# Kernel optimization log

Hardware: AMD Instinct MI355X
Metric: run time of the kernel (lower is better)

Reference implementation:

```python
import jax, jax.numpy as jnp
import numpy as np

D_MODEL = 2048
NUM_HEADS = 16
D_K = D_MODEL // NUM_HEADS
B, S = 2, 2048


def setup_inputs() -> dict:
    key = jax.random.key(0)
    ks = jax.random.split(key, 9)
    sc = 1.0 / np.sqrt(D_MODEL)
    x = jax.random.normal(ks[0], (B, S, D_MODEL), dtype=jnp.float32)
    # broadcastable causal mask [1,1,S,S]; mask==0 positions get -inf
    mask = jnp.tril(jnp.ones((S, S), dtype=jnp.int32))[None, None]
    wq = jax.random.normal(ks[1], (D_MODEL, D_MODEL), dtype=jnp.float32) * sc
    bq = jax.random.normal(ks[2], (D_MODEL,), dtype=jnp.float32) * 0.01
    wk = jax.random.normal(ks[3], (D_MODEL, D_MODEL), dtype=jnp.float32) * sc
    bk = jax.random.normal(ks[4], (D_MODEL,), dtype=jnp.float32) * 0.01
    wv = jax.random.normal(ks[5], (D_MODEL, D_MODEL), dtype=jnp.float32) * sc
    bv = jax.random.normal(ks[6], (D_MODEL,), dtype=jnp.float32) * 0.01
    wo = jax.random.normal(ks[7], (D_MODEL, D_MODEL), dtype=jnp.float32) * sc
    bo = jax.random.normal(ks[8], (D_MODEL,), dtype=jnp.float32) * 0.01
    return {"x": x, "wq": wq, "bq": bq, "wk": wk, "bk": bk,
            "wv": wv, "bv": bv, "wo": wo, "bo": bo, "mask": mask}


def reference(x, wq, bq, wk, bk, wv, bv, wo, bo, mask):
    b, s, _ = x.shape
    # nn.Linear computes x @ W.T + b; weights stored [out, in]
    def proj(w, bias):
        y = jnp.einsum('bsd,ed->bse', x, w) + bias
        return y.reshape(b, s, NUM_HEADS, D_K).transpose(0, 2, 1, 3)  # [b,h,s,dk]
    q = proj(wq, bq)
    k = proj(wk, bk)
    v = proj(wv, bv)
    scores = jnp.einsum('bhid,bhjd->bhij', q, k) / jnp.sqrt(jnp.float32(D_K))
    scores = jnp.where(mask == 0, -jnp.inf, scores)
    attn = jax.nn.softmax(scores, axis=-1)  # dropout p=0.0 -> identity
    out = jnp.einsum('bhij,bhjd->bhid', attn, v)
    out = out.transpose(0, 2, 1, 3).reshape(b, s, D_MODEL)
    return jnp.einsum('bsd,ed->bse', out, wo) + bo
```

## Files before the change

kernel.cpp:

```cpp
#include <hip/hip_runtime.h>
#include <cstdint>
#include <cstddef>

typedef __attribute__((ext_vector_type(8))) short bf16x8;
typedef __attribute__((ext_vector_type(8))) unsigned short u16x8;
typedef __attribute__((ext_vector_type(4))) unsigned short u16x4;
typedef __attribute__((ext_vector_type(2))) unsigned u32x2;
typedef __attribute__((ext_vector_type(4))) float f32x4;

#define MFMA16(A, B, C) __builtin_amdgcn_mfma_f32_16x16x32_bf16((A), (B), (C), 0, 0, 0)

__device__ __forceinline__ unsigned short f2bf(float f) {
  unsigned u = __builtin_bit_cast(unsigned, f);
  u += 0x7FFFu + ((u >> 16) & 1u);
  return (unsigned short)(u >> 16);
}
__device__ __forceinline__ unsigned packbf2(float lo, float hi) {
  unsigned ul = __builtin_bit_cast(unsigned, lo);
  unsigned uh = __builtin_bit_cast(unsigned, hi);
  ul += 0x7FFFu + ((ul >> 16) & 1u);
  uh += 0x7FFFu + ((uh >> 16) & 1u);
  return (ul >> 16) | (uh & 0xffff0000u);
}

__device__ __forceinline__ void gload_lds16(const void* gsrc, void* ldst) {
  __builtin_amdgcn_global_load_lds(
      (const __attribute__((address_space(1))) unsigned int*)gsrc,
      (__attribute__((address_space(3))) unsigned int*)ldst,
      16, 0, 0);
}

__global__ __launch_bounds__(256) void cvt_all(
    const float* __restrict__ sx, const float* __restrict__ s1,
    const float* __restrict__ s2, const float* __restrict__ s3,
    const float* __restrict__ s4,
    unsigned short* __restrict__ dx, unsigned short* __restrict__ d1,
    unsigned short* __restrict__ d2, unsigned short* __restrict__ d3,
    unsigned short* __restrict__ d4) {
  const int y = blockIdx.y;
  const float* src;
  unsigned short* dst;
  if (y == 0)      { src = sx;               dst = dx; }
  else if (y == 1) { src = sx + (1u << 22);  dst = dx + (1u << 22); }
  else if (y == 2) { src = s1; dst = d1; }
  else if (y == 3) { src = s2; dst = d2; }
  else if (y == 4) { src = s3; dst = d3; }
  else             { src = s4; dst = d4; }
  const size_t i = ((size_t)blockIdx.x * 256 + threadIdx.x) * 4;
  f32x4 v = *(const f32x4*)(src + i);
  u16x4 o;
  o[0] = f2bf(v[0]); o[1] = f2bf(v[1]); o[2] = f2bf(v[2]); o[3] = f2bf(v[3]);
  *(u16x4*)(dst + i) = o;
}

template <int MODE>
__device__ __forceinline__ void gemm8_tile(const unsigned short* __restrict__ A,
                                           const unsigned short* __restrict__ W,
                                           const float* __restrict__ bias,
                                           void* __restrict__ C,
                                           int bx, int by) {
  constexpr int K = 2048, N = 2048;
  constexpr int NT = K / 64;
  __shared__ __align__(16) unsigned short lA[3][256 * 64];
  __shared__ __align__(16) unsigned short lB[3][128 * 64];
  const int tid = threadIdx.x;
  const int lane = tid & 63;
  const int w = tid >> 6;
  const int g = lane >> 4;
  const int l15 = lane & 15;
  const int wm = w >> 1, wn = w & 1;
  const int m0 = by * 256, n0 = bx * 128;

  auto stageA = [&](int kt, int buf) {
    const int kb = kt * 64;
#pragma unroll
    for (int it = 0; it < 4; ++it) {
      const int f = it * 512 + tid;
      const int r = f >> 3, s = f & 7;
      gload_lds16(A + (size_t)(m0 + r) * K + kb + ((s * 8) ^ ((r & 7) << 3)),
                  (char*)&lA[buf][0] + (it * 512 + w * 64) * 16);
    }
  };
  auto stageB = [&](int kt, int buf) {
    const int kb = kt * 64;
#pragma unroll
    for (int it = 0; it < 2; ++it) {
      const int f = it * 512 + tid;
      const int r = f >> 3, s = f & 7;
      gload_lds16(W + (size_t)(n0 + r) * K + kb + ((s * 8) ^ ((r & 7) << 3)),
                  (char*)&lB[buf][0] + (it * 512 + w * 64) * 16);
    }
  };

  f32x4 acc[4][4];
#pragma unroll
  for (int i = 0; i < 4; ++i)
#pragma unroll
    for (int j = 0; j < 4; ++j) acc[i][j] = f32x4{0.f, 0.f, 0.f, 0.f};

  stageA(0, 0); stageB(0, 0);
  stageA(1, 1); stageB(1, 1);
  asm volatile("s_waitcnt vmcnt(6)" ::: "memory");
  __builtin_amdgcn_s_barrier();
  __builtin_amdgcn_sched_barrier(0);

  int cur = 0, nxt = 2;
  for (int kt = 0; kt < NT; ++kt) {
    const unsigned short* As = &lA[cur][0];
    const unsigned short* Bs = &lB[cur][0];
    bf16x8 bfr[4][2], af[4][2];
#pragma unroll
    for (int ni = 0; ni < 4; ++ni) {
      const int rb = wn * 64 + ni * 16 + l15;
#pragma unroll
      for (int kh = 0; kh < 2; ++kh)
        bfr[ni][kh] =
            *(const bf16x8*)&Bs[rb * 64 + ((kh * 32 + g * 8) ^ ((rb & 7) << 3))];
    }
#pragma unroll
    for (int mi = 0; mi < 4; ++mi) {
      const int ra = wm * 64 + mi * 16 + l15;
#pragma unroll
      for (int kh = 0; kh < 2; ++kh)
        af[mi][kh] =
            *(const bf16x8*)&As[ra * 64 + ((kh * 32 + g * 8) ^ ((ra & 7) << 3))];
    }
    if (kt + 2 < NT) { stageA(kt + 2, nxt); stageB(kt + 2, nxt); }
    __builtin_amdgcn_s_setprio(1);
#pragma unroll
    for (int kh = 0; kh < 2; ++kh)
#pragma unroll
      for (int mi = 0; mi < 4; ++mi)
#pragma unroll
        for (int ni = 0; ni < 4; ++ni)
          acc[mi][ni] = MFMA16(af[mi][kh], bfr[ni][kh], acc[mi][ni]);
    __builtin_amdgcn_s_setprio(0);
    if (kt < NT - 2)       asm volatile("s_waitcnt vmcnt(6)" ::: "memory");
    else if (kt == NT - 2) asm volatile("s_waitcnt vmcnt(0)" ::: "memory");
    __builtin_amdgcn_s_barrier();
    __builtin_amdgcn_sched_barrier(0);
    cur = (cur == 2) ? 0 : cur + 1;
    nxt = (nxt == 2) ? 0 : nxt + 1;
  }

  if (MODE == 0) {
#pragma unroll
    for (int ni = 0; ni < 4; ++ni) {
      const int n = n0 + wn * 64 + ni * 16 + l15;
      const float bval = bias[n];
#pragma unroll
      for (int mi = 0; mi < 4; ++mi) {
        const int mb = m0 + wm * 64 + mi * 16 + g * 4;
#pragma unroll
        for (int r = 0; r < 4; ++r)
          ((float*)C)[(size_t)(mb + r) * N + n] = acc[mi][ni][r] + bval;
      }
    }
  } else {
    unsigned short* lc = &lA[0][0];
#pragma unroll
    for (int ni = 0; ni < 4; ++ni) {
      const int n = n0 + wn * 64 + ni * 16 + l15;
      const float bval = bias[n];
      const int col = wn * 64 + ni * 16 + l15;
#pragma unroll
      for (int mi = 0; mi < 4; ++mi) {
        const int rbase = wm * 64 + mi * 16 + g * 4;
#pragma unroll
        for (int r = 0; r < 4; ++r)
          lc[(rbase + r) * 128 + col] = f2bf(acc[mi][ni][r] + bval);
      }
    }
    __syncthreads();
    const int bb = m0 >> 11;
    const int hh = n0 >> 7;
    unsigned short* dst = (unsigned short*)C +
        (((size_t)(bb * 16 + hh) * 2048) + (m0 & 2047)) * 128;
#pragma unroll
    for (int p = 0; p < 8; ++p) {
      const int f = p * 512 + tid;
      const int row = f >> 4, slot = f & 15;
      *(u16x8*)(dst + (size_t)row * 128 + slot * 8) =
          *(const u16x8*)&lc[row * 128 + slot * 8];
    }
  }
}

__global__ __launch_bounds__(512, 2) void gemm_qkv(
    const unsigned short* __restrict__ x,
    const unsigned short* __restrict__ wq, const float* __restrict__ bq,
    const unsigned short* __restrict__ wk, const float* __restrict__ bk,
    const unsigned short* __restrict__ wv, const float* __restrict__ bv,
    unsigned short* __restrict__ qo, unsigned short* __restrict__ ko,
    unsigned short* __restrict__ vo) {
  const int o = blockIdx.x + ((int)blockIdx.y << 4) + ((int)blockIdx.z << 8);
  const int t = (o & 7) * 96 + (o >> 3);
  const int z = t >> 8;
  const int by = (t & 255) >> 4;
  const int bx = t & 15;
  const unsigned short* W = (z == 0) ? wq : (z == 1) ? wk : wv;
  const float* B = (z == 0) ? bq : (z == 1) ? bk : bv;
  unsigned short* O = (z == 0) ? qo : (z == 1) ? ko : vo;
  gemm8_tile<1>(x, W, B, O, bx, by);
}

__global__ __launch_bounds__(512, 2) void gemm_out(
    const unsigned short* __restrict__ A, const unsigned short* __restrict__ wo,
    const float* __restrict__ bo, float* __restrict__ C) {
  const int o = blockIdx.x + ((int)blockIdx.y << 4);
  const int t = (o & 7) * 32 + (o >> 3);
  const int by = t >> 4;
  const int bx = t & 15;
  gemm8_tile<0>(A, wo, bo, C, bx, by);
}

__global__ __launch_bounds__(256, 2) void attn_fwd(
    const unsigned short* __restrict__ Q, const unsigned short* __restrict__ K,
    const unsigned short* __restrict__ V, unsigned short* __restrict__ O) {
  __shared__ unsigned short lK[2][64 * 128];
  __shared__ unsigned short lV[128 * 72];
  __shared__ unsigned short lP[4][32 * 72];
  const int tid = threadIdx.x;
  const int lane = tid & 63;
  const int w = tid >> 6;
  const int g = lane >> 4;
  const int l15 = lane & 15;
  const int bx = blockIdx.x;
  const int bh = blockIdx.y;
  const int qb = (bh >= 16) ? (15 - bx) : bx;
  const int nt = 2 * qb + 2;
  const size_t head_off = (size_t)bh * 2048 * 128;
  const unsigned short* Qh = Q + head_off;
  const unsigned short* Kh = K + head_off;
  const unsigned short* Vh = V + head_off;

  bf16x8 qf[2][4];
#pragma unroll
  for (int mi = 0; mi < 2; ++mi) {
    const int row = qb * 128 + w * 32 + mi * 16 + l15;
#pragma unroll
    for (int ks = 0; ks < 4; ++ks) {
      const int s = ks * 4 + g;
      qf[mi][ks] = *(const bf16x8*)(Qh + (size_t)row * 128 + s * 8);
    }
  }

  const int vj0 = (tid & 31) * 2;
  const int vd0 = (tid >> 5) * 16;
  u16x8 vr[4];

  auto stageK = [&](int t, int buf) {
#pragma unroll
    for (int it = 0; it < 4; ++it) {
      const int f = it * 256 + tid;
      const int r = f >> 4, s = f & 15;
      const int sc = s ^ (r & 7);
      gload_lds16(Kh + (size_t)(t * 64 + r) * 128 + sc * 8,
                  (char*)&lK[buf][0] + (it * 256 + w * 64) * 16);
    }
  };
  auto loadV = [&](int t) {
    const unsigned short* vp = Vh + (size_t)(t * 64 + vj0) * 128 + vd0;
    vr[0] = *(const u16x8*)(vp);
    vr[1] = *(const u16x8*)(vp + 8);
    vr[2] = *(const u16x8*)(vp + 128);
    vr[3] = *(const u16x8*)(vp + 136);
  };
  auto writeV = [&]() {
#pragma unroll
    for (int dd = 0; dd < 8; ++dd) {
      unsigned pk0 = (unsigned)vr[0][dd] | ((unsigned)vr[2][dd] << 16);
      unsigned pk1 = (unsigned)vr[1][dd] | ((unsigned)vr[3][dd] << 16);
      *(unsigned*)&lV[(vd0 + dd) * 72 + vj0] = pk0;
      *(unsigned*)&lV[(vd0 + 8 + dd) * 72 + vj0] = pk1;
    }
  };

  loadV(0);
  stageK(0, 0);
  writeV();
  __syncthreads();

  f32x4 acc_o[2][8];
#pragma unroll
  for (int mi = 0; mi < 2; ++mi)
#pragma unroll
    for (int i = 0; i < 8; ++i) acc_o[mi][i] = f32x4{0.f, 0.f, 0.f, 0.f};
  float mrun[2], lrun[2];
#pragma unroll
  for (int mi = 0; mi < 2; ++mi) { mrun[mi] = -__builtin_inff(); lrun[mi] = 0.f; }

  const float SL2E = 0.12751744f;
  const int qrow0 = qb * 128 + w * 32;

  int cur = 0;
  for (int t = 0; t < nt; ++t) {
    const int kv0 = t * 64;
    const bool pre = (t + 1 < nt);
    if (pre) { loadV(t + 1); stageK(t + 1, cur ^ 1); }

    const bool active = (kv0 <= qrow0 + 31);
    if (active) {
      const unsigned short* lKc = &lK[cur][0];
      f32x4 sacc[4][2];
#pragma unroll
      for (int jb = 0; jb < 4; ++jb) {
        sacc[jb][0] = f32x4{0.f, 0.f, 0.f, 0.f};
        sacc[jb][1] = f32x4{0.f, 0.f, 0.f, 0.f};
      }
      __builtin_amdgcn_s_setprio(1);
#pragma unroll
      for (int jb = 0; jb < 4; ++jb) {
        const int r = jb * 16 + l15;
#pragma unroll
        for (int ks = 0; ks < 4; ++ks) {
          const int s = ks * 4 + g;
          bf16x8 kf = *(const bf16x8*)&lKc[r * 128 + (s ^ (r & 7)) * 8];
          sacc[jb][0] = MFMA16(kf, qf[0][ks], sacc[jb][0]);
          sacc[jb][1] = MFMA16(kf, qf[1][ks], sacc[jb][1]);
        }
      }
      __builtin_amdgcn_s_setprio(0);

      const bool need_mask = (kv0 + 63 >= qrow0);
      float psc_l[2];
      bool defer_mi[2];
#pragma unroll
      for (int mi = 0; mi < 2; ++mi) {
        const int icol = qrow0 + mi * 16 + l15;
        f32x4 pe[4];
#pragma unroll
        for (int jb = 0; jb < 4; ++jb) {
#pragma unroll
          for (int rr = 0; rr < 4; ++rr) {
            float tv = sacc[jb][mi][rr] * SL2E;
            if (need_mask && (kv0 + jb * 16 + g * 4 + rr > icol))
              tv = -__builtin_inff();
            pe[jb][rr] = tv;
          }
        }
        f32x4 m4 = f32x4{fmaxf(fmaxf(pe[0][0], pe[1][0]), fmaxf(pe[2][0], pe[3][0])),
                         fmaxf(fmaxf(pe[0][1], pe[1][1]), fmaxf(pe[2][1], pe[3][1])),
                         fmaxf(fmaxf(pe[0][2], pe[1][2]), fmaxf(pe[2][2], pe[3][2])),
                         fmaxf(fmaxf(pe[0][3], pe[1][3]), fmaxf(pe[2][3], pe[3][3]))};
        float mx = fmaxf(fmaxf(m4[0], m4[1]), fmaxf(m4[2], m4[3]));
        mx = fmaxf(mx, __shfl_xor(mx, 16));
        mx = fmaxf(mx, __shfl_xor(mx, 32));
        const bool dfr = (__all(mx - mrun[mi] <= 8.0f) != 0);
        defer_mi[mi] = dfr;
        if (dfr) {
          psc_l[mi] = 1.0f;
        } else {
          const float mnew = fmaxf(mrun[mi], mx);
          psc_l[mi] = exp2f(mrun[mi] - mnew);
          mrun[mi] = mnew;
        }
        float rs = 0.f;
#pragma unroll
        for (int jb = 0; jb < 4; ++jb) {
#pragma unroll
          for (int rr = 0; rr < 4; ++rr) {
            const float e = exp2f(pe[jb][rr] - mrun[mi]);
            pe[jb][rr] = e;
            rs += e;
          }
        }
        rs += __shfl_xor(rs, 16);
        rs += __shfl_xor(rs, 32);
        lrun[mi] = lrun[mi] * psc_l[mi] + rs;
#pragma unroll
        for (int jb = 0; jb < 4; ++jb) {
          u32x2 pw;
          pw[0] = packbf2(pe[jb][0], pe[jb][1]);
          pw[1] = packbf2(pe[jb][2], pe[jb][3]);
          *(u32x2*)&lP[w][(mi * 16 + l15) * 72 + jb * 16 + g * 4] = pw;
        }
      }
      __builtin_amdgcn_sched_barrier(0);

#pragma unroll
      for (int mi = 0; mi < 2; ++mi) {
        if (!defer_mi[mi]) {
          float psc_pv[4];
#pragma unroll
          for (int r = 0; r < 4; ++r)
            psc_pv[r] = __shfl(psc_l[mi], g * 4 + r);
#pragma unroll
          for (int nb = 0; nb < 8; ++nb)
#pragma unroll
            for (int r = 0; r < 4; ++r) acc_o[mi][nb][r] *= psc_pv[r];
        }
      }

      bf16x8 pa[2][2];
#pragma unroll
      for (int mi = 0; mi < 2; ++mi)
#pragma unroll
        for (int h = 0; h < 2; ++h)
          pa[mi][h] = *(const bf16x8*)&lP[w][(mi * 16 + l15) * 72 + h * 32 + g * 8];
      __builtin_amdgcn_s_setprio(1);
#pragma unroll
      for (int nb = 0; nb < 8; ++nb) {
        const int vrow = nb * 16 + l15;
#pragma unroll
        for (int h = 0; h < 2; ++h) {
          bf16x8 vf = *(const bf16x8*)&lV[vrow * 72 + h * 32 + g * 8];
          acc_o[0][nb] = MFMA16(pa[0][h], vf, acc_o[0][nb]);
          acc_o[1][nb] = MFMA16(pa[1][h], vf, acc_o[1][nb]);
        }
      }
      __builtin_amdgcn_s_setprio(0);
    }

    __syncthreads();
    if (pre) writeV();
    __syncthreads();
    cur ^= 1;
  }

  const int b = bh >> 4, hh = bh & 15;
  float linv[2][4];
#pragma unroll
  for (int mi = 0; mi < 2; ++mi)
#pragma unroll
    for (int r = 0; r < 4; ++r)
      linv[mi][r] = 1.0f / __shfl(lrun[mi], g * 4 + r);
#pragma unroll
  for (int mi = 0; mi < 2; ++mi)
#pragma unroll
    for (int nb = 0; nb < 8; ++nb)
#pragma unroll
      for (int r = 0; r < 4; ++r) {
        const int i = qb * 128 + w * 32 + mi * 16 + g * 4 + r;
        const float o = acc_o[mi][nb][r] * linv[mi][r];
        O[((size_t)(b * 2048 + i)) * 2048 + hh * 128 + nb * 16 + l15] = f2bf(o);
      }
}

extern "C" void kernel_launch(void* const* d_in, const int* in_sizes, int n_in,
                              void* d_out, int out_size, void* d_ws, size_t ws_size,
                              hipStream_t stream) {
  const float* x  = (const float*)d_in[0];
  const float* wq = (const float*)d_in[1];
  const float* bq = (const float*)d_in[2];
  const float* wk = (const float*)d_in[3];
  const float* bk = (const float*)d_in[4];
  const float* wv = (const float*)d_in[5];
  const float* bv = (const float*)d_in[6];
  const float* wo = (const float*)d_in[7];
  const float* bo = (const float*)d_in[8];

  const size_t NX = (size_t)2 * 2048 * 2048;
  const size_t NW = (size_t)2048 * 2048;
  const size_t need = (NX + 4 * NW + 3 * NX) * sizeof(unsigned short);
  if (ws_size < need) return;
  unsigned short* xbf  = (unsigned short*)d_ws;
  unsigned short* wqb  = xbf + NX;
  unsigned short* wkb  = wqb + NW;
  unsigned short* wvb  = wkb + NW;
  unsigned short* wob  = wvb + NW;
  unsigned short* qbuf = wob + NW;
  unsigned short* kbuf = qbuf + NX;
  unsigned short* vbuf = kbuf + NX;
  unsigned short* aobuf = xbf;

  cvt_all<<<dim3(4096, 6), 256, 0, stream>>>(x, wq, wk, wv, wo,
                                             xbf, wqb, wkb, wvb, wob);
  gemm_qkv<<<dim3(16, 16, 3), 512, 0, stream>>>(xbf, wqb, bq, wkb, bk, wvb, bv,
                                                qbuf, kbuf, vbuf);
  attn_fwd<<<dim3(16, 32), 256, 0, stream>>>(qbuf, kbuf, vbuf, aobuf);
  gemm_out<<<dim3(16, 16), 512, 0, stream>>>(aobuf, wob, bo, (float*)d_out);
}
```

Before: 267.6 us.

## Redistribute softmax probabilities via cross-lane shuffles instead of LDS staging

Removes the per-wave LDS buffer used to transpose the bf16 probability tile between the QK and PV MFMA layouts, and rebuilds the PV A-operand with ds_bpermute shuffles plus selects. This frees LDS and lets the launch bound target 3 blocks per CU instead of 2. The trade-off is 16 shuffles per 32-row chunk and extra register pressure, which a tighter launch bound may force into spills.

Measured after the change: 360.5 us. 34.7% more time.

```diff
diff --git a/kernel.cpp b/kernel.cpp
--- a/kernel.cpp
+++ b/kernel.cpp
@@ -5,7 +5,7 @@
 typedef __attribute__((ext_vector_type(8))) short bf16x8;
 typedef __attribute__((ext_vector_type(8))) unsigned short u16x8;
 typedef __attribute__((ext_vector_type(4))) unsigned short u16x4;
-typedef __attribute__((ext_vector_type(2))) unsigned u32x2;
+typedef __attribute__((ext_vector_type(4))) unsigned u32x4;
 typedef __attribute__((ext_vector_type(4))) float f32x4;
 
 #define MFMA16(A, B, C) __builtin_amdgcn_mfma_f32_16x16x32_bf16((A), (B), (C), 0, 0, 0)
@@ -214,12 +214,11 @@
   gemm8_tile<0>(A, wo, bo, C, bx, by);
 }
 
-__global__ __launch_bounds__(256, 2) void attn_fwd(
+__global__ __launch_bounds__(256, 3) void attn_fwd(
     const unsigned short* __restrict__ Q, const unsigned short* __restrict__ K,
     const unsigned short* __restrict__ V, unsigned short* __restrict__ O) {
   __shared__ unsigned short lK[2][64 * 128];
   __shared__ unsigned short lV[128 * 72];
-  __shared__ unsigned short lP[4][32 * 72];
   const int tid = threadIdx.x;
   const int lane = tid & 63;
   const int w = tid >> 6;
@@ -292,6 +291,9 @@
 
   const float SL2E = 0.12751744f;
   const int qrow0 = qb * 128 + w * 32;
+  const int srcA = l15 + 16 * ((2 * g) & 3);
+  const int srcB = l15 + 16 * ((2 * g + 1) & 3);
+  const bool ghi = (g & 2) != 0;
 
   int cur = 0;
   for (int t = 0; t < nt; ++t) {
@@ -325,6 +327,7 @@
       const bool need_mask = (kv0 + 63 >= qrow0);
       float psc_l[2];
       bool defer_mi[2];
+      unsigned pws[2][4][2];
 #pragma unroll
       for (int mi = 0; mi < 2; ++mi) {
         const int icol = qrow0 + mi * 16 + l15;
@@ -370,13 +373,10 @@
         lrun[mi] = lrun[mi] * psc_l[mi] + rs;
 #pragma unroll
         for (int jb = 0; jb < 4; ++jb) {
-          u32x2 pw;
-          pw[0] = packbf2(pe[jb][0], pe[jb][1]);
-          pw[1] = packbf2(pe[jb][2], pe[jb][3]);
-          *(u32x2*)&lP[w][(mi * 16 + l15) * 72 + jb * 16 + g * 4] = pw;
-        }
-      }
-      __builtin_amdgcn_sched_barrier(0);
+          pws[mi][jb][0] = packbf2(pe[jb][0], pe[jb][1]);
+          pws[mi][jb][1] = packbf2(pe[jb][2], pe[jb][3]);
+        }
+      }
 
 #pragma unroll
       for (int mi = 0; mi < 2; ++mi) {
@@ -394,10 +394,26 @@
 
       bf16x8 pa[2][2];
 #pragma unroll
-      for (int mi = 0; mi < 2; ++mi)
-#pragma unroll
-        for (int h = 0; h < 2; ++h)
-          pa[mi][h] = *(const bf16x8*)&lP[w][(mi * 16 + l15) * 72 + h * 32 + g * 8];
+      for (int mi = 0; mi < 2; ++mi) {
+#pragma unroll
+        for (int h = 0; h < 2; ++h) {
+          const unsigned a0 = __shfl(pws[mi][2 * h][0], srcA);
+          const unsigned a1 = __shfl(pws[mi][2 * h][1], srcA);
+          const unsigned a2 = __shfl(pws[mi][2 * h][0], srcB);
+          const unsigned a3 = __shfl(pws[mi][2 * h][1], srcB);
+          const unsigned b0 = __shfl(pws[mi][2 * h + 1][0], srcA);
+          const unsigned b1 = __shfl(pws[mi][2 * h + 1][1], srcA);
+          const unsigned b2 = __shfl(pws[mi][2 * h + 1][0], srcB);
+          const unsigned b3 = __shfl(pws[mi][2 * h + 1][1], srcB);
+          u32x4 wv;
+          wv[0] = ghi ? b0 : a0;
+          wv[1] = ghi ? b1 : a1;
+          wv[2] = ghi ? b2 : a2;
+          wv[3] = ghi ? b3 : a3;
+          pa[mi][h] = __builtin_bit_cast(bf16x8, wv);
+        }
+      }
+
       __builtin_amdgcn_s_setprio(1);
 #pragma unroll
       for (int nb = 0; nb < 8; ++nb) {
```

## Double-buffer V tile in LDS and drop one barrier per attention iteration

Applied to the files above, without the earlier changes.

The transposed V tile now lives in two LDS buffers indexed by iteration parity, so the next tile is written right after the current PV compute and only one __syncthreads per loop step remains instead of two. Padded row strides (72) for V and P are replaced with unpadded 64-element rows using an XOR swizzle to avoid LDS bank conflicts. LDS use per block grows by one V buffer, which may limit occupancy at two blocks per CU.

Measured after the change: 265.5 us (median of 2 runs). Within noise of the previous version (-0.8%).

```diff
diff --git a/kernel.cpp b/kernel.cpp
--- a/kernel.cpp
+++ b/kernel.cpp
@@ -218,8 +218,8 @@
     const unsigned short* __restrict__ Q, const unsigned short* __restrict__ K,
     const unsigned short* __restrict__ V, unsigned short* __restrict__ O) {
   __shared__ unsigned short lK[2][64 * 128];
-  __shared__ unsigned short lV[128 * 72];
-  __shared__ unsigned short lP[4][32 * 72];
+  __shared__ unsigned short lV[2][128 * 64];
+  __shared__ unsigned short lP[4][32 * 64];
   const int tid = threadIdx.x;
   const int lane = tid & 63;
   const int w = tid >> 6;
@@ -266,19 +266,21 @@
     vr[2] = *(const u16x8*)(vp + 128);
     vr[3] = *(const u16x8*)(vp + 136);
   };
-  auto writeV = [&]() {
+  auto writeV = [&](int buf) {
+    unsigned short* lVb = &lV[buf][0];
 #pragma unroll
     for (int dd = 0; dd < 8; ++dd) {
+      const int sj = vj0 ^ (dd << 3);
       unsigned pk0 = (unsigned)vr[0][dd] | ((unsigned)vr[2][dd] << 16);
       unsigned pk1 = (unsigned)vr[1][dd] | ((unsigned)vr[3][dd] << 16);
-      *(unsigned*)&lV[(vd0 + dd) * 72 + vj0] = pk0;
-      *(unsigned*)&lV[(vd0 + 8 + dd) * 72 + vj0] = pk1;
+      *(unsigned*)&lVb[(vd0 + dd) * 64 + sj] = pk0;
+      *(unsigned*)&lVb[(vd0 + 8 + dd) * 64 + sj] = pk1;
     }
   };
 
   loadV(0);
   stageK(0, 0);
-  writeV();
+  writeV(0);
   __syncthreads();
 
   f32x4 acc_o[2][8];
@@ -293,15 +295,15 @@
   const float SL2E = 0.12751744f;
   const int qrow0 = qb * 128 + w * 32;
 
-  int cur = 0;
   for (int t = 0; t < nt; ++t) {
     const int kv0 = t * 64;
     const bool pre = (t + 1 < nt);
-    if (pre) { loadV(t + 1); stageK(t + 1, cur ^ 1); }
+    if (pre) { loadV(t + 1); stageK(t + 1, (t + 1) & 1); }
 
     const bool active = (kv0 <= qrow0 + 31);
     if (active) {
-      const unsigned short* lKc = &lK[cur][0];
+      const unsigned short* lKc = &lK[t & 1][0];
+      const unsigned short* lVc = &lV[t & 1][0];
       f32x4 sacc[4][2];
 #pragma unroll
       for (int jb = 0; jb < 4; ++jb) {
@@ -373,7 +375,8 @@
           u32x2 pw;
           pw[0] = packbf2(pe[jb][0], pe[jb][1]);
           pw[1] = packbf2(pe[jb][2], pe[jb][3]);
-          *(u32x2*)&lP[w][(mi * 16 + l15) * 72 + jb * 16 + g * 4] = pw;
+          *(u32x2*)&lP[w][(mi * 16 + l15) * 64 +
+                          ((jb * 16 + g * 4) ^ ((l15 & 7) << 3))] = pw;
         }
       }
       __builtin_amdgcn_sched_barrier(0);
@@ -397,14 +400,16 @@
       for (int mi = 0; mi < 2; ++mi)
 #pragma unroll
         for (int h = 0; h < 2; ++h)
-          pa[mi][h] = *(const bf16x8*)&lP[w][(mi * 16 + l15) * 72 + h * 32 + g * 8];
+          pa[mi][h] = *(const bf16x8*)&lP[w][(mi * 16 + l15) * 64 +
+                                            ((h * 32 + g * 8) ^ ((l15 & 7) << 3))];
       __builtin_amdgcn_s_setprio(1);
 #pragma unroll
       for (int nb = 0; nb < 8; ++nb) {
         const int vrow = nb * 16 + l15;
 #pragma unroll
         for (int h = 0; h < 2; ++h) {
-          bf16x8 vf = *(const bf16x8*)&lV[vrow * 72 + h * 32 + g * 8];
+          bf16x8 vf = *(const bf16x8*)&lVc[vrow * 64 +
+                                           ((h * 32 + g * 8) ^ ((vrow & 7) << 3))];
           acc_o[0][nb] = MFMA16(pa[0][h], vf, acc_o[0][nb]);
           acc_o[1][nb] = MFMA16(pa[1][h], vf, acc_o[1][nb]);
         }
@@ -412,10 +417,8 @@
       __builtin_amdgcn_s_setprio(0);
     }
 
+    if (pre) writeV((t + 1) & 1);
     __syncthreads();
-    if (pre) writeV();
-    __syncthreads();
-    cur ^= 1;
   }
 
   const int b = bh >> 4, hh = bh & 15;
```
